# Performance work log

Hardware: AMD Instinct MI355X
Metric: run time of the kernel (lower is better)

Reference implementation:

```python
import jax, jax.numpy as jnp
import numpy as np

B, S = 32, 2048
NUM_SKILL = 4096
D = 64   # dim_s
M = 32   # size_m


def setup_inputs() -> dict:
    key = jax.random.key(0)
    ks = jax.random.split(key, 16)
    he = (2.0 / D) ** 0.5  # kaiming-normal-ish scale
    return {
        "question": jax.random.randint(ks[0], (B, S), 0, NUM_SKILL),
        "response": jax.random.randint(ks[1], (B, S), 0, 2),
        "skill": jax.random.randint(ks[2], (B, S), 0, NUM_SKILL),
        "mask": jnp.ones((B, S), jnp.float32),
        "k_c_emb": jax.random.normal(ks[3], (NUM_SKILL, D), jnp.float32) * 0.05,
        "v_c_emb": jax.random.normal(ks[4], (2 * NUM_SKILL, D), jnp.float32) * 0.05,
        "Mk": jax.random.normal(ks[5], (M, D), jnp.float32) * he,
        "Mv0": jax.random.normal(ks[6], (M, D), jnp.float32) * he,
        "e_W": jax.random.normal(ks[7], (D, D), jnp.float32) * he,
        "e_b": jnp.zeros((D,), jnp.float32),
        "a_W": jax.random.normal(ks[8], (D, D), jnp.float32) * he,
        "a_b": jnp.zeros((D,), jnp.float32),
        "f_W": jax.random.normal(ks[9], (2 * D, D), jnp.float32) * (2.0 / (2 * D)) ** 0.5,
        "f_b": jnp.zeros((D,), jnp.float32),
        "p_W": jax.random.normal(ks[10], (D, 1), jnp.float32) * he,
        "p_b": jnp.zeros((1,), jnp.float32),
    }


def reference(question, response, skill, mask, k_c_emb, v_c_emb, Mk, Mv0,
              e_W, e_b, a_W, a_b, f_W, f_b, p_W, p_b):
    num_skill = k_c_emb.shape[0]
    batch = question.shape[0]

    xc = skill + num_skill * response          # [B,S]
    k = k_c_emb[skill]                         # [B,S,D]
    v = v_c_emb[xc]                            # [B,S,D]

    w = jax.nn.softmax(jnp.einsum('bsd,md->bsm', k, Mk), axis=-1)  # [B,S,M]
    e = jax.nn.sigmoid(v @ e_W + e_b)          # [B,S,D]
    a = jnp.tanh(v @ a_W + a_b)                # [B,S,D]

    def step(Mvt, inp):
        wt, et, at, mt = inp                   # [B,M],[B,D],[B,D],[B]
        Mvt_next = Mvt * (1.0 - wt[:, :, None] * et[:, None, :]) \
                   + wt[:, :, None] * at[:, None, :]
        Mvt = jnp.where(mt[:, None, None] == 1, Mvt_next, Mvt)
        return Mvt, Mvt

    xs = (jnp.swapaxes(w, 0, 1), jnp.swapaxes(e, 0, 1),
          jnp.swapaxes(a, 0, 1), jnp.swapaxes(mask, 0, 1))
    Mv_init = jnp.broadcast_to(Mv0[None], (batch, M, D))
    _, Mv_states = jax.lax.scan(step, Mv_init, xs)   # [S,B,M,D]; Mv_states[t] = Mv after t+1 updates

    # Mv[:,1:-1] in torch = states after 1..S-1 updates = Mv_states[0:S-1]
    Mv_used = jnp.swapaxes(Mv_states[:-1], 0, 1)      # [B,S-1,M,D]
    read = jnp.einsum('bsm,bsmd->bsd', w[:, 1:], Mv_used)  # [B,S-1,D]
    f = jnp.tanh(jnp.concatenate([read, k[:, 1:]], axis=-1) @ f_W + f_b)
    # dropout is identity in eval mode
    p = (f @ p_W + p_b).squeeze(-1)                   # [B,S-1]
    return p
```

## Files before the change

kernel.cpp:

```cpp
#include <hip/hip_runtime.h>
#include <hip/hip_bf16.h>
#include <math.h>

#define BB 32
#define SS 2048
#define DD 64
#define MM 32
#define NSKILL 4096
#define CC 64
#define LL 32
#define NOUT (BB * (SS - 1))

__device__ __forceinline__ float sigmoidf_(float x) {
    return 1.f / (1.f + __expf(-x));
}
__device__ __forceinline__ float tanhf_(float x) {
    float t = __expf(-2.f * fabsf(x));
    float r = (1.f - t) / (1.f + t);
    return copysignf(r, x);
}

__global__ __launch_bounds__(256) void k_prep(
    const float* __restrict__ eW, const float* __restrict__ aW,
    const float* __restrict__ fW,
    float* __restrict__ eWt, float* __restrict__ aWt, float* __restrict__ fWt,
    float* __restrict__ outz)
{
    const int t = blockIdx.x * 256 + threadIdx.x;
    if (t < DD * DD) {
        const int i = t >> 6, d = t & 63;
        eWt[d * DD + i] = eW[i * DD + d];
        aWt[d * DD + i] = aW[i * DD + d];
    }
    {
        const int i = t >> 6, d = t & 63;
        fWt[d * 128 + i] = fW[i * DD + d];
    }
    for (int i = t; i < NOUT; i += 8192) outz[i] = 0.f;
}

__global__ __launch_bounds__(64, 2) void k_token(
    const int* __restrict__ skill, const int* __restrict__ resp,
    const float* __restrict__ k_emb, const float* __restrict__ v_emb,
    const float* __restrict__ Mk,
    const float* __restrict__ eWt, const float* __restrict__ eb,
    const float* __restrict__ aWt, const float* __restrict__ ab,
    float* __restrict__ w_out, float* __restrict__ e_out, float* __restrict__ a_out)
{
    __shared__ float stg[64 * 33];
    const int lane = threadIdx.x;
    const int role = blockIdx.x % 5;
    const int g    = blockIdx.x / 5;
    const int tok  = g * 64 + lane;
    const int sk   = skill[tok];

    if (role == 0) {
        float4 kq[16];
        const float4* kp = (const float4*)(k_emb + (size_t)sk * DD);
        #pragma unroll
        for (int q = 0; q < 16; ++q) kq[q] = kp[q];

        float lg[MM];
        #pragma unroll
        for (int m = 0; m < MM; ++m) {
            const float* mk = Mk + m * DD;
            float a0 = 0.f, a1 = 0.f, a2 = 0.f, a3 = 0.f;
            #pragma unroll
            for (int q = 0; q < 16; ++q) {
                const float4 kv = kq[q];
                a0 = fmaf(kv.x, mk[4*q+0], a0);
                a1 = fmaf(kv.y, mk[4*q+1], a1);
                a2 = fmaf(kv.z, mk[4*q+2], a2);
                a3 = fmaf(kv.w, mk[4*q+3], a3);
            }
            lg[m] = (a0 + a1) + (a2 + a3);
        }
        float mx = lg[0];
        #pragma unroll
        for (int m = 1; m < MM; ++m) mx = fmaxf(mx, lg[m]);
        float sm = 0.f;
        #pragma unroll
        for (int m = 0; m < MM; ++m) { lg[m] = __expf(lg[m] - mx); sm += lg[m]; }
        const float inv = 1.f / sm;

        #pragma unroll
        for (int m = 0; m < MM; ++m) stg[lane * 33 + m] = lg[m] * inv;
        __syncthreads();
        float* wo = w_out + (size_t)g * 64 * MM;
        #pragma unroll 8
        for (int i = 0; i < 32; ++i) {
            const int idx = i * 64 + lane;
            wo[idx] = stg[(idx >> 5) * 33 + (idx & 31)];
        }
    } else {
        const bool isE = (role <= 2);
        const int  dh  = (role & 1) ? 0 : 1;
        const float* Wt   = isE ? eWt : aWt;
        const float* bias = isE ? eb  : ab;
        float*       op   = isE ? e_out : a_out;

        const int xc = sk + NSKILL * resp[tok];
        float4 vq[16];
        const float4* vp = (const float4*)(v_emb + (size_t)xc * DD);
        #pragma unroll
        for (int q = 0; q < 16; ++q) vq[q] = vp[q];

        const int d0 = dh * 32;
        for (int dd = 0; dd < 32; dd += 2) {
            const float* c0 = Wt + (d0 + dd) * DD;
            const float* c1 = c0 + DD;
            float x0 = bias[d0 + dd], x1 = bias[d0 + dd + 1];
            #pragma unroll
            for (int q = 0; q < 16; ++q) {
                const float4 vv = vq[q];
                x0 = fmaf(vv.x, c0[4*q+0], x0); x0 = fmaf(vv.y, c0[4*q+1], x0);
                x0 = fmaf(vv.z, c0[4*q+2], x0); x0 = fmaf(vv.w, c0[4*q+3], x0);
                x1 = fmaf(vv.x, c1[4*q+0], x1); x1 = fmaf(vv.y, c1[4*q+1], x1);
                x1 = fmaf(vv.z, c1[4*q+2], x1); x1 = fmaf(vv.w, c1[4*q+3], x1);
            }
            if (isE) { x0 = sigmoidf_(x0); x1 = sigmoidf_(x1); }
            else     { x0 = tanhf_(x0);    x1 = tanhf_(x1);    }
            stg[lane * 33 + dd]     = x0;
            stg[lane * 33 + dd + 1] = x1;
        }
        __syncthreads();
        #pragma unroll 8
        for (int i = 0; i < 32; ++i) {
            const int idx = i * 64 + lane;
            const int row = idx >> 5, col = idx & 31;
            op[(size_t)(g * 64 + row) * DD + d0 + col] = stg[row * 33 + col];
        }
    }
}

__global__ __launch_bounds__(64, 4) void k_pass1(
    const float* __restrict__ w, const float* __restrict__ mask,
    const float* __restrict__ e, const float* __restrict__ a,
    float* __restrict__ Abar, float* __restrict__ Bbar)
{
    __shared__ float4 wl[LL * 16 / 4];
    const int lane = threadIdx.x;
    const int bc = blockIdx.x >> 1;
    const int mh = blockIdx.x & 1;
    const int b = bc / CC;
    const int c = bc % CC;
    const int t0 = c * LL;

    const float4* wg = (const float4*)(w + (size_t)(b * SS + t0) * MM);
    #pragma unroll
    for (int u = 0; u < 2; ++u) {
        const int q4 = u * 64 + lane;
        const int j = q4 >> 2;
        const int q = q4 & 3;
        const float s = (mask[b * SS + t0 + j] == 1.f) ? 1.f : 0.f;
        float4 wq = wg[j * 8 + mh * 4 + q];
        wq.x *= s; wq.y *= s; wq.z *= s; wq.w *= s;
        wl[q4] = wq;
    }
    __syncthreads();

    float Ab[16], Bb[16];
    #pragma unroll
    for (int i = 0; i < 16; ++i) { Ab[i] = 1.f; Bb[i] = 0.f; }

    const float* ep = e + (size_t)(b * SS + t0) * DD + lane;
    const float* ap = a + (size_t)(b * SS + t0) * DD + lane;
    for (int j = 0; j < LL; ++j) {
        const float ed = ep[j * DD];
        const float ad = ap[j * DD];
        const float4* wlj = wl + j * 4;
        #pragma unroll
        for (int u = 0; u < 4; ++u) {
            const float4 wq = wlj[u];
            float t1;
            t1 = fmaf(-wq.x, ed, 1.f); Ab[4*u+0] *= t1; Bb[4*u+0] = fmaf(Bb[4*u+0], t1, wq.x * ad);
            t1 = fmaf(-wq.y, ed, 1.f); Ab[4*u+1] *= t1; Bb[4*u+1] = fmaf(Bb[4*u+1], t1, wq.y * ad);
            t1 = fmaf(-wq.z, ed, 1.f); Ab[4*u+2] *= t1; Bb[4*u+2] = fmaf(Bb[4*u+2], t1, wq.z * ad);
            t1 = fmaf(-wq.w, ed, 1.f); Ab[4*u+3] *= t1; Bb[4*u+3] = fmaf(Bb[4*u+3], t1, wq.w * ad);
        }
    }
    float* Ao = Abar + (size_t)bc * MM * DD + (size_t)(mh * 16) * DD + lane;
    float* Bo = Bbar + (size_t)bc * MM * DD + (size_t)(mh * 16) * DD + lane;
    #pragma unroll
    for (int i = 0; i < 16; ++i) { Ao[i * DD] = Ab[i]; Bo[i * DD] = Bb[i]; }
}

__global__ __launch_bounds__(256, 2) void k_pass2(
    const float* __restrict__ Abar, float* __restrict__ Bbar_cst,
    const float* __restrict__ Mv0)
{
    const int idx = blockIdx.x * 256 + threadIdx.x;
    const int b = idx >> 11;
    const int md = idx & 2047;
    float s = Mv0[md];
    for (int c = 0; c < CC; ++c) {
        const int off = ((b * CC + c) << 11) + md;
        const float sa = Abar[off];
        const float sb = Bbar_cst[off];
        Bbar_cst[off] = s;
        s = fmaf(s, sa, sb);
    }
}

__global__ __launch_bounds__(64, 4) void k_pass3(
    const float* __restrict__ w, const float* __restrict__ mask,
    const float* __restrict__ e, const float* __restrict__ a,
    const float* __restrict__ cstate, float* __restrict__ readv)
{
    __shared__ float4 wl[LL * MM / 4];
    __shared__ float4 wn[LL * MM / 4];
    const int lane = threadIdx.x;
    const int bc = blockIdx.x >> 1;
    const int dh = blockIdx.x & 1;
    const int b = bc / CC;
    const int c = bc % CC;
    const int t0 = c * LL;
    const bool last = (c == CC - 1);
    const int dof = lane & 31;
    const int mh  = lane >> 5;

    const float4* wg  = (const float4*)(w + (size_t)(b * SS + t0) * MM);
    const float4* wg2 = (const float4*)(w + (size_t)(b * SS + t0 + 1) * MM);
    #pragma unroll
    for (int u = 0; u < 4; ++u) {
        const int q4 = u * 64 + lane;
        const int j = q4 >> 3;
        const float s = (mask[b * SS + t0 + j] == 1.f) ? 1.f : 0.f;
        float4 wq = wg[q4];
        wq.x *= s; wq.y *= s; wq.z *= s; wq.w *= s;
        wl[q4] = wq;
        float4 wq2;
        if (last && q4 >= 248) wq2 = make_float4(0.f, 0.f, 0.f, 0.f);
        else                   wq2 = wg2[q4];
        wn[q4] = wq2;
    }
    __syncthreads();

    float Mv[16];
    const float* cs = cstate + (size_t)bc * MM * DD + (size_t)(mh * 16) * DD
                      + dh * 32 + dof;
    #pragma unroll
    for (int i = 0; i < 16; ++i) Mv[i] = cs[i * DD];

    const float* ep = e + (size_t)(b * SS + t0) * DD + dh * 32 + dof;
    const float* ap = a + (size_t)(b * SS + t0) * DD + dh * 32 + dof;
    float* ro = readv + (size_t)(b * SS + t0 + 1) * DD + dh * 32 + dof;
    for (int j = 0; j < LL; ++j) {
        const float ed = ep[j * DD];
        const float ad = ap[j * DD];
        const float4* wlj = wl + j * 8 + mh * 4;
        const float4* wnj = wn + j * 8 + mh * 4;
        float r0 = 0.f, r1 = 0.f, r2 = 0.f, r3 = 0.f;
        #pragma unroll
        for (int u = 0; u < 4; ++u) {
            const float4 wq = wlj[u];
            const float4 w2 = wnj[u];
            float t1;
            t1 = fmaf(-wq.x, ed, 1.f); Mv[4*u+0] = fmaf(Mv[4*u+0], t1, wq.x * ad); r0 = fmaf(w2.x, Mv[4*u+0], r0);
            t1 = fmaf(-wq.y, ed, 1.f); Mv[4*u+1] = fmaf(Mv[4*u+1], t1, wq.y * ad); r1 = fmaf(w2.y, Mv[4*u+1], r1);
            t1 = fmaf(-wq.z, ed, 1.f); Mv[4*u+2] = fmaf(Mv[4*u+2], t1, wq.z * ad); r2 = fmaf(w2.z, Mv[4*u+2], r2);
            t1 = fmaf(-wq.w, ed, 1.f); Mv[4*u+3] = fmaf(Mv[4*u+3], t1, wq.w * ad); r3 = fmaf(w2.w, Mv[4*u+3], r3);
        }
        float r = (r0 + r1) + (r2 + r3);
        r += __shfl_xor(r, 32);
        if (mh == 0 && !(last && j == LL - 1))
            ro[j * DD] = r;
    }
}

__global__ __launch_bounds__(64, 2) void k_final(
    const float* __restrict__ readv, const int* __restrict__ skill,
    const float* __restrict__ k_emb,
    const float* __restrict__ fWt, const float* __restrict__ fb,
    const float* __restrict__ pW, const float* __restrict__ pb,
    float* __restrict__ out)
{
    const int lane = threadIdx.x;
    const int o  = (blockIdx.x >> 1) * 64 + lane;
    const int dh = blockIdx.x & 1;
    const bool valid = o < NOUT;
    const int oc = valid ? o : 0;
    const int b = oc / (SS - 1);
    const int s = oc - b * (SS - 1) + 1;
    const size_t tok = (size_t)b * SS + s;

    float4 rq[16], kq[16];
    const float4* rp = (const float4*)(readv + tok * DD);
    const float4* kp = (const float4*)(k_emb + (size_t)skill[tok] * DD);
    #pragma unroll
    for (int q = 0; q < 16; ++q) { rq[q] = rp[q]; kq[q] = kp[q]; }

    float pacc = 0.f;
    const int d0 = dh * 32;
    for (int dd = 0; dd < 32; dd += 2) {
        const float* c0 = fWt + (d0 + dd) * 128;
        const float* c1 = c0 + 128;
        float f0 = fb[d0 + dd], f1 = fb[d0 + dd + 1];
        #pragma unroll
        for (int q = 0; q < 16; ++q) {
            const float4 rv = rq[q];
            f0 = fmaf(rv.x, c0[4*q+0], f0); f0 = fmaf(rv.y, c0[4*q+1], f0);
            f0 = fmaf(rv.z, c0[4*q+2], f0); f0 = fmaf(rv.w, c0[4*q+3], f0);
            f1 = fmaf(rv.x, c1[4*q+0], f1); f1 = fmaf(rv.y, c1[4*q+1], f1);
            f1 = fmaf(rv.z, c1[4*q+2], f1); f1 = fmaf(rv.w, c1[4*q+3], f1);
        }
        #pragma unroll
        for (int q = 0; q < 16; ++q) {
            const float4 kv = kq[q];
            f0 = fmaf(kv.x, c0[64+4*q+0], f0); f0 = fmaf(kv.y, c0[64+4*q+1], f0);
            f0 = fmaf(kv.z, c0[64+4*q+2], f0); f0 = fmaf(kv.w, c0[64+4*q+3], f0);
            f1 = fmaf(kv.x, c1[64+4*q+0], f1); f1 = fmaf(kv.y, c1[64+4*q+1], f1);
            f1 = fmaf(kv.z, c1[64+4*q+2], f1); f1 = fmaf(kv.w, c1[64+4*q+3], f1);
        }
        pacc = fmaf(tanhf_(f0), pW[d0 + dd], pacc);
        pacc = fmaf(tanhf_(f1), pW[d0 + dd + 1], pacc);
    }
    if (valid) atomicAdd(&out[o], pacc + (dh ? 0.f : pb[0]));
}

extern "C" void kernel_launch(void* const* d_in, const int* in_sizes, int n_in,
                              void* d_out, int out_size, void* d_ws, size_t ws_size,
                              hipStream_t stream)
{
    const int*   response = (const int*)d_in[1];
    const int*   skill    = (const int*)d_in[2];
    const float* mask     = (const float*)d_in[3];
    const float* k_emb    = (const float*)d_in[4];
    const float* v_emb    = (const float*)d_in[5];
    const float* Mk       = (const float*)d_in[6];
    const float* Mv0      = (const float*)d_in[7];
    const float* eW       = (const float*)d_in[8];
    const float* ebias    = (const float*)d_in[9];
    const float* aW       = (const float*)d_in[10];
    const float* abias    = (const float*)d_in[11];
    const float* fW       = (const float*)d_in[12];
    const float* fbias    = (const float*)d_in[13];
    const float* pW       = (const float*)d_in[14];
    const float* pbias    = (const float*)d_in[15];
    float* out = (float*)d_out;

    float* ws    = (float*)d_ws;
    float* w_    = ws;
    float* e_    = w_    + (size_t)BB * SS * MM;
    float* a_    = e_    + (size_t)BB * SS * DD;
    float* Abar  = a_    + (size_t)BB * SS * DD;
    float* Bbar  = Abar  + (size_t)BB * CC * MM * DD;
    float* readv = Bbar  + (size_t)BB * CC * MM * DD;
    float* eWt   = readv + (size_t)BB * SS * DD;
    float* aWt   = eWt   + DD * DD;
    float* fWt   = aWt   + DD * DD;

    k_prep <<<32,   256, 0, stream>>>(eW, aW, fW, eWt, aWt, fWt, out);
    k_token<<<5120,  64, 0, stream>>>(skill, response, k_emb, v_emb, Mk,
                                      eWt, ebias, aWt, abias, w_, e_, a_);
    k_pass1<<<BB * CC * 2, 64, 0, stream>>>(w_, mask, e_, a_, Abar, Bbar);
    k_pass2<<<256,  256, 0, stream>>>(Abar, Bbar, Mv0);
    k_pass3<<<BB * CC * 2, 64, 0, stream>>>(w_, mask, e_, a_, Bbar, readv);
    k_final<<<2048,  64, 0, stream>>>(readv, skill, k_emb, fWt, fbias,
                                      pW, pbias, out);
}
```

Measured before the change: 232.1 us.

## Restructure per-token kernels to keep weights in registers and stage tokens in LDS

Replaces the prep and token kernels with two 256-thread kernels: one computes the softmax address weights, with one lane per memory slot and a shuffle-based softmax, and the other computes e and a, with one lane per output dimension and weight columns held in registers. Token embeddings are staged in shared memory and broadcast across lanes. The final kernel is reorganised the same way: f_W columns live in registers, the output dot product is reduced with wave shuffles, and results are written directly instead of through atomics, so the output zeroing pass and the weight transposes are dropped. This aims to cut redundant weight loads and uncoalesced stores, at the cost of heavy register pressure, up to 128 floats per thread, that may limit occupancy or spill.

```diff
diff --git a/kernel.cpp b/kernel.cpp
--- a/kernel.cpp
+++ b/kernel.cpp
@@ -20,116 +20,102 @@
     return copysignf(r, x);
 }
 
-__global__ __launch_bounds__(256) void k_prep(
-    const float* __restrict__ eW, const float* __restrict__ aW,
-    const float* __restrict__ fW,
-    float* __restrict__ eWt, float* __restrict__ aWt, float* __restrict__ fWt,
-    float* __restrict__ outz)
-{
-    const int t = blockIdx.x * 256 + threadIdx.x;
-    if (t < DD * DD) {
-        const int i = t >> 6, d = t & 63;
-        eWt[d * DD + i] = eW[i * DD + d];
-        aWt[d * DD + i] = aW[i * DD + d];
-    }
-    {
-        const int i = t >> 6, d = t & 63;
-        fWt[d * 128 + i] = fW[i * DD + d];
-    }
-    for (int i = t; i < NOUT; i += 8192) outz[i] = 0.f;
-}
-
-__global__ __launch_bounds__(64, 2) void k_token(
+__global__ __launch_bounds__(256, 2) void k_w(
+    const int* __restrict__ skill, const float* __restrict__ k_emb,
+    const float* __restrict__ Mk, float* __restrict__ w_out)
+{
+    __shared__ float kst[64][64];
+    const int tid = threadIdx.x;
+    const int g = blockIdx.x;
+    #pragma unroll
+    for (int p = 0; p < 4; ++p) {
+        const int r = p * 16 + (tid >> 4);
+        const int t = g * 64 + r;
+        const float4 kv = ((const float4*)(k_emb + (size_t)skill[t] * DD))[tid & 15];
+        *(float4*)&kst[r][(tid & 15) * 4] = kv;
+    }
+    const int l  = tid & 63;
+    const int m  = l & 31;
+    const int th = l >> 5;
+    const int w  = tid >> 6;
+    float4 mk4[16];
+    const float4* mkp = (const float4*)(Mk + m * DD);
+    #pragma unroll
+    for (int q = 0; q < 16; ++q) mk4[q] = mkp[q];
+    __syncthreads();
+
+    for (int j = 0; j < 8; ++j) {
+        const int tl = w * 16 + j * 2 + th;
+        const float4* kp = (const float4*)&kst[tl][0];
+        float a0 = 0.f, a1 = 0.f, a2 = 0.f, a3 = 0.f;
+        #pragma unroll
+        for (int q = 0; q < 16; ++q) {
+            const float4 kv = kp[q];
+            a0 = fmaf(kv.x, mk4[q].x, a0);
+            a1 = fmaf(kv.y, mk4[q].y, a1);
+            a2 = fmaf(kv.z, mk4[q].z, a2);
+            a3 = fmaf(kv.w, mk4[q].w, a3);
+        }
+        const float lg = (a0 + a1) + (a2 + a3);
+        float mx = lg;
+        #pragma unroll
+        for (int off = 16; off >= 1; off >>= 1) mx = fmaxf(mx, __shfl_xor(mx, off));
+        const float ev = __expf(lg - mx);
+        float sm = ev;
+        #pragma unroll
+        for (int off = 16; off >= 1; off >>= 1) sm += __shfl_xor(sm, off);
+        w_out[(size_t)(g * 64 + tl) * MM + m] = ev / sm;
+    }
+}
+
+__global__ __launch_bounds__(256, 2) void k_ea(
     const int* __restrict__ skill, const int* __restrict__ resp,
-    const float* __restrict__ k_emb, const float* __restrict__ v_emb,
-    const float* __restrict__ Mk,
-    const float* __restrict__ eWt, const float* __restrict__ eb,
-    const float* __restrict__ aWt, const float* __restrict__ ab,
-    float* __restrict__ w_out, float* __restrict__ e_out, float* __restrict__ a_out)
-{
-    __shared__ float stg[64 * 33];
-    const int lane = threadIdx.x;
-    const int role = blockIdx.x % 5;
-    const int g    = blockIdx.x / 5;
-    const int tok  = g * 64 + lane;
-    const int sk   = skill[tok];
-
-    if (role == 0) {
-        float4 kq[16];
-        const float4* kp = (const float4*)(k_emb + (size_t)sk * DD);
-        #pragma unroll
-        for (int q = 0; q < 16; ++q) kq[q] = kp[q];
-
-        float lg[MM];
-        #pragma unroll
-        for (int m = 0; m < MM; ++m) {
-            const float* mk = Mk + m * DD;
-            float a0 = 0.f, a1 = 0.f, a2 = 0.f, a3 = 0.f;
-            #pragma unroll
-            for (int q = 0; q < 16; ++q) {
-                const float4 kv = kq[q];
-                a0 = fmaf(kv.x, mk[4*q+0], a0);
-                a1 = fmaf(kv.y, mk[4*q+1], a1);
-                a2 = fmaf(kv.z, mk[4*q+2], a2);
-                a3 = fmaf(kv.w, mk[4*q+3], a3);
-            }
-            lg[m] = (a0 + a1) + (a2 + a3);
-        }
-        float mx = lg[0];
-        #pragma unroll
-        for (int m = 1; m < MM; ++m) mx = fmaxf(mx, lg[m]);
-        float sm = 0.f;
-        #pragma unroll
-        for (int m = 0; m < MM; ++m) { lg[m] = __expf(lg[m] - mx); sm += lg[m]; }
-        const float inv = 1.f / sm;
-
-        #pragma unroll
-        for (int m = 0; m < MM; ++m) stg[lane * 33 + m] = lg[m] * inv;
-        __syncthreads();
-        float* wo = w_out + (size_t)g * 64 * MM;
-        #pragma unroll 8
-        for (int i = 0; i < 32; ++i) {
-            const int idx = i * 64 + lane;
-            wo[idx] = stg[(idx >> 5) * 33 + (idx & 31)];
-        }
-    } else {
-        const bool isE = (role <= 2);
-        const int  dh  = (role & 1) ? 0 : 1;
-        const float* Wt   = isE ? eWt : aWt;
-        const float* bias = isE ? eb  : ab;
-        float*       op   = isE ? e_out : a_out;
-
-        const int xc = sk + NSKILL * resp[tok];
-        float4 vq[16];
-        const float4* vp = (const float4*)(v_emb + (size_t)xc * DD);
-        #pragma unroll
-        for (int q = 0; q < 16; ++q) vq[q] = vp[q];
-
-        const int d0 = dh * 32;
-        for (int dd = 0; dd < 32; dd += 2) {
-            const float* c0 = Wt + (d0 + dd) * DD;
-            const float* c1 = c0 + DD;
-            float x0 = bias[d0 + dd], x1 = bias[d0 + dd + 1];
-            #pragma unroll
-            for (int q = 0; q < 16; ++q) {
-                const float4 vv = vq[q];
-                x0 = fmaf(vv.x, c0[4*q+0], x0); x0 = fmaf(vv.y, c0[4*q+1], x0);
-                x0 = fmaf(vv.z, c0[4*q+2], x0); x0 = fmaf(vv.w, c0[4*q+3], x0);
-                x1 = fmaf(vv.x, c1[4*q+0], x1); x1 = fmaf(vv.y, c1[4*q+1], x1);
-                x1 = fmaf(vv.z, c1[4*q+2], x1); x1 = fmaf(vv.w, c1[4*q+3], x1);
-            }
-            if (isE) { x0 = sigmoidf_(x0); x1 = sigmoidf_(x1); }
-            else     { x0 = tanhf_(x0);    x1 = tanhf_(x1);    }
-            stg[lane * 33 + dd]     = x0;
-            stg[lane * 33 + dd + 1] = x1;
-        }
-        __syncthreads();
-        #pragma unroll 8
-        for (int i = 0; i < 32; ++i) {
-            const int idx = i * 64 + lane;
-            const int row = idx >> 5, col = idx & 31;
-            op[(size_t)(g * 64 + row) * DD + d0 + col] = stg[row * 33 + col];
-        }
+    const float* __restrict__ v_emb,
+    const float* __restrict__ eW, const float* __restrict__ eb,
+    const float* __restrict__ aW, const float* __restrict__ ab,
+    float* __restrict__ e_out, float* __restrict__ a_out)
+{
+    __shared__ float vst[64][64];
+    const int tid = threadIdx.x;
+    const int g = blockIdx.x;
+    #pragma unroll
+    for (int p = 0; p < 4; ++p) {
+        const int r = p * 16 + (tid >> 4);
+        const int t = g * 64 + r;
+        const int xc = skill[t] + NSKILL * resp[t];
+        const float4 vv = ((const float4*)(v_emb + (size_t)xc * DD))[tid & 15];
+        *(float4*)&vst[r][(tid & 15) * 4] = vv;
+    }
+    const int l = tid & 63;
+    const int w = tid >> 6;
+    float ew[64], aw[64];
+    #pragma unroll
+    for (int i = 0; i < 64; ++i) ew[i] = eW[i * DD + l];
+    #pragma unroll
+    for (int i = 0; i < 64; ++i) aw[i] = aW[i * DD + l];
+    const float ebd = eb[l], abd = ab[l];
+    __syncthreads();
+
+    for (int j = 0; j < 16; ++j) {
+        const int tl = w * 16 + j;
+        const float4* vp = (const float4*)&vst[tl][0];
+        float e0 = ebd, e1 = 0.f, e2 = 0.f, e3 = 0.f;
+        float x0 = abd, x1 = 0.f, x2 = 0.f, x3 = 0.f;
+        #pragma unroll
+        for (int q = 0; q < 16; ++q) {
+            const float4 vv = vp[q];
+            e0 = fmaf(vv.x, ew[4*q+0], e0);
+            e1 = fmaf(vv.y, ew[4*q+1], e1);
+            e2 = fmaf(vv.z, ew[4*q+2], e2);
+            e3 = fmaf(vv.w, ew[4*q+3], e3);
+            x0 = fmaf(vv.x, aw[4*q+0], x0);
+            x1 = fmaf(vv.y, aw[4*q+1], x1);
+            x2 = fmaf(vv.z, aw[4*q+2], x2);
+            x3 = fmaf(vv.w, aw[4*q+3], x3);
+        }
+        const size_t t = (size_t)(g * 64 + tl);
+        e_out[t * DD + l] = sigmoidf_((e0 + e1) + (e2 + e3));
+        a_out[t * DD + l] = tanhf_((x0 + x1) + (x2 + x3));
     }
 }
 
@@ -268,54 +254,69 @@
     }
 }
 
-__global__ __launch_bounds__(64, 2) void k_final(
+__global__ __launch_bounds__(256, 2) void k_final(
     const float* __restrict__ readv, const int* __restrict__ skill,
     const float* __restrict__ k_emb,
-    const float* __restrict__ fWt, const float* __restrict__ fb,
+    const float* __restrict__ fW, const float* __restrict__ fb,
     const float* __restrict__ pW, const float* __restrict__ pb,
     float* __restrict__ out)
 {
-    const int lane = threadIdx.x;
-    const int o  = (blockIdx.x >> 1) * 64 + lane;
-    const int dh = blockIdx.x & 1;
-    const bool valid = o < NOUT;
-    const int oc = valid ? o : 0;
-    const int b = oc / (SS - 1);
-    const int s = oc - b * (SS - 1) + 1;
-    const size_t tok = (size_t)b * SS + s;
-
-    float4 rq[16], kq[16];
-    const float4* rp = (const float4*)(readv + tok * DD);
-    const float4* kp = (const float4*)(k_emb + (size_t)skill[tok] * DD);
-    #pragma unroll
-    for (int q = 0; q < 16; ++q) { rq[q] = rp[q]; kq[q] = kp[q]; }
-
-    float pacc = 0.f;
-    const int d0 = dh * 32;
-    for (int dd = 0; dd < 32; dd += 2) {
-        const float* c0 = fWt + (d0 + dd) * 128;
-        const float* c1 = c0 + 128;
-        float f0 = fb[d0 + dd], f1 = fb[d0 + dd + 1];
+    __shared__ float rst[64][64];
+    __shared__ float kst[64][64];
+    __shared__ float pbuf[64];
+    const int tid = threadIdx.x;
+    const int g = blockIdx.x;
+    #pragma unroll
+    for (int p = 0; p < 4; ++p) {
+        const int r = p * 16 + (tid >> 4);
+        int o = g * 64 + r;
+        if (o >= NOUT) o = 0;
+        const int b = o / (SS - 1);
+        const int s = o - b * (SS - 1) + 1;
+        const size_t tok = (size_t)b * SS + s;
+        const int q = tid & 15;
+        *(float4*)&rst[r][q * 4] = ((const float4*)(readv + tok * DD))[q];
+        *(float4*)&kst[r][q * 4] = ((const float4*)(k_emb + (size_t)skill[tok] * DD))[q];
+    }
+    const int l = tid & 63;
+    const int w = tid >> 6;
+    float fw[128];
+    #pragma unroll
+    for (int i = 0; i < 128; ++i) fw[i] = fW[i * DD + l];
+    const float fbd = fb[l], pwd = pW[l];
+    __syncthreads();
+
+    for (int j = 0; j < 16; ++j) {
+        const int tl = w * 16 + j;
+        const float4* rp = (const float4*)&rst[tl][0];
+        const float4* kp = (const float4*)&kst[tl][0];
+        float f0 = fbd, f1 = 0.f, f2 = 0.f, f3 = 0.f;
         #pragma unroll
         for (int q = 0; q < 16; ++q) {
-            const float4 rv = rq[q];
-            f0 = fmaf(rv.x, c0[4*q+0], f0); f0 = fmaf(rv.y, c0[4*q+1], f0);
-            f0 = fmaf(rv.z, c0[4*q+2], f0); f0 = fmaf(rv.w, c0[4*q+3], f0);
-            f1 = fmaf(rv.x, c1[4*q+0], f1); f1 = fmaf(rv.y, c1[4*q+1], f1);
-            f1 = fmaf(rv.z, c1[4*q+2], f1); f1 = fmaf(rv.w, c1[4*q+3], f1);
+            const float4 rv = rp[q];
+            f0 = fmaf(rv.x, fw[4*q+0], f0);
+            f1 = fmaf(rv.y, fw[4*q+1], f1);
+            f2 = fmaf(rv.z, fw[4*q+2], f2);
+            f3 = fmaf(rv.w, fw[4*q+3], f3);
         }
         #pragma unroll
         for (int q = 0; q < 16; ++q) {
-            const float4 kv = kq[q];
-            f0 = fmaf(kv.x, c0[64+4*q+0], f0); f0 = fmaf(kv.y, c0[64+4*q+1], f0);
-            f0 = fmaf(kv.z, c0[64+4*q+2], f0); f0 = fmaf(kv.w, c0[64+4*q+3], f0);
-            f1 = fmaf(kv.x, c1[64+4*q+0], f1); f1 = fmaf(kv.y, c1[64+4*q+1], f1);
-            f1 = fmaf(kv.z, c1[64+4*q+2], f1); f1 = fmaf(kv.w, c1[64+4*q+3], f1);
-        }
-        pacc = fmaf(tanhf_(f0), pW[d0 + dd], pacc);
-        pacc = fmaf(tanhf_(f1), pW[d0 + dd + 1], pacc);
-    }
-    if (valid) atomicAdd(&out[o], pacc + (dh ? 0.f : pb[0]));
+            const float4 kv = kp[q];
+            f0 = fmaf(kv.x, fw[64+4*q+0], f0);
+            f1 = fmaf(kv.y, fw[64+4*q+1], f1);
+            f2 = fmaf(kv.z, fw[64+4*q+2], f2);
+            f3 = fmaf(kv.w, fw[64+4*q+3], f3);
+        }
+        float pv = tanhf_((f0 + f1) + (f2 + f3)) * pwd;
+        #pragma unroll
+        for (int off = 32; off >= 1; off >>= 1) pv += __shfl_xor(pv, off);
+        if (l == 0) pbuf[tl] = pv;
+    }
+    __syncthreads();
+    if (tid < 64) {
+        const int o = g * 64 + tid;
+        if (o < NOUT) out[o] = pbuf[tid] + pb[0];
+    }
 }
 
 extern "C" void kernel_launch(void* const* d_in, const int* in_sizes, int n_in,
@@ -346,16 +347,13 @@
     float* Abar  = a_    + (size_t)BB * SS * DD;
     float* Bbar  = Abar  + (size_t)BB * CC * MM * DD;
     float* readv = Bbar  + (size_t)BB * CC * MM * DD;
-    float* eWt   = readv + (size_t)BB * SS * DD;
-    float* aWt   = eWt   + DD * DD;
-    float* fWt   = aWt   + DD * DD;
-
-    k_prep <<<32,   256, 0, stream>>>(eW, aW, fW, eWt, aWt, fWt, out);
-    k_token<<<5120,  64, 0, stream>>>(skill, response, k_emb, v_emb, Mk,
-                                      eWt, ebias, aWt, abias, w_, e_, a_);
+
+    k_w    <<<1024, 256, 0, stream>>>(skill, k_emb, Mk, w_);
+    k_ea   <<<1024, 256, 0, stream>>>(skill, response, v_emb,
+                                      eW, ebias, aW, abias, e_, a_);
     k_pass1<<<BB * CC * 2, 64, 0, stream>>>(w_, mask, e_, a_, Abar, Bbar);
     k_pass2<<<256,  256, 0, stream>>>(Abar, Bbar, Mv0);
     k_pass3<<<BB * CC * 2, 64, 0, stream>>>(w_, mask, e_, a_, Bbar, readv);
-    k_final<<<2048,  64, 0, stream>>>(readv, skill, k_emb, fWt, fbias,
+    k_final<<<1024, 256, 0, stream>>>(readv, skill, k_emb, fW, fbias,
                                       pW, pbias, out);
 }
```

Result: faster. 216.1 us (-6.9%).
